# Kernel tuning notes

Measured on AMD Instinct MI355X. Metric: run time of the kernel, lower is better.

The kernel has to match this reference:

```python
import jax, jax.numpy as jnp
import numpy as np

B, T, D = 2, 2048, 512
H, W = 8, 32
d = D // H


def setup_inputs() -> dict:
    key = jax.random.key(0)
    ks = jax.random.split(key, 9)
    s = 1.0 / np.sqrt(D)
    return {
        "x": jax.random.normal(ks[0], (B, T, D), dtype=jnp.float32),
        "wq": jax.random.normal(ks[1], (D, D), dtype=jnp.float32) * s,
        "bq": jnp.zeros((D,), dtype=jnp.float32),
        "wk": jax.random.normal(ks[2], (D, D), dtype=jnp.float32) * s,
        "bk": jnp.zeros((D,), dtype=jnp.float32),
        "wv": jax.random.normal(ks[3], (D, D), dtype=jnp.float32) * s,
        "bv": jnp.zeros((D,), dtype=jnp.float32),
        "wo": jax.random.normal(ks[4], (D, D), dtype=jnp.float32) * s,
        "bo": jnp.zeros((D,), dtype=jnp.float32),
    }


def _local_attn(x, wq, bq, wk, bk, wv, bv, wo, bo):
    Bx, Tx, Dx = x.shape
    # projections (weights stored as [D_in, D_out])
    Q = (x @ wq + bq).reshape(Bx, Tx, H, d).transpose(0, 2, 1, 3)  # [B,H,T,d]
    K = (x @ wk + bk).reshape(Bx, Tx, H, d).transpose(0, 2, 1, 3)
    V = (x @ wv + bv).reshape(Bx, Tx, H, d).transpose(0, 2, 1, 3)
    # zero-pad time axis by W on both sides (matches F.pad value=0; NO masking,
    # padded zero keys get score 0 and participate in softmax like the original)
    Kp = jnp.pad(K, ((0, 0), (0, 0), (W, W), (0, 0)))  # [B,H,T+2W,d]
    Vp = jnp.pad(V, ((0, 0), (0, 0), (W, W), (0, 0)))
    idx = jnp.arange(Tx)[:, None] + jnp.arange(2 * W + 1)[None, :]  # [T, 2W+1]
    K_loc = Kp[:, :, idx, :]  # [B,H,T,2W+1,d]
    V_loc = Vp[:, :, idx, :]
    scores = jnp.einsum("bhtd,bhtwd->bhtw", Q, K_loc) / jnp.sqrt(jnp.asarray(d, x.dtype))
    attn = jax.nn.softmax(scores, axis=-1)
    out = jnp.einsum("bhtw,bhtwd->bhtd", attn, V_loc)  # [B,H,T,d]
    out = out.transpose(0, 2, 1, 3).reshape(Bx, Tx, Dx)
    return out @ wo + bo


def reference(x, wq, bq, wk, bk, wv, bv, wo, bo):
    return _local_attn(x, wq, bq, wk, bk, wv, bv, wo, bo)
```

## Files before the change

kernel.cpp:

```cpp
#include <hip/hip_runtime.h>

using f16x8 = __attribute__((ext_vector_type(8))) _Float16;
using f16x4 = __attribute__((ext_vector_type(4))) _Float16;
using f32x4 = __attribute__((ext_vector_type(4))) float;

#define T_SEQ 2048
#define D_MODEL 512
#define NH 8
#define HD 64
#define NB 2
#define M_ROWS (NB * T_SEQ)

#define GLOAD_LDS16(g, l)                                              \
  __builtin_amdgcn_global_load_lds(                                    \
      (const __attribute__((address_space(1))) void*)(g),              \
      (__attribute__((address_space(3))) void*)(l), 16, 0, 0)

__global__ __launch_bounds__(256) void cvt_w(
    const float* __restrict__ wq, const float* __restrict__ wk,
    const float* __restrict__ wv, const float* __restrict__ wo,
    const float* __restrict__ bq, const float* __restrict__ bk,
    const float* __restrict__ bv, _Float16* __restrict__ wT,
    float* __restrict__ bias3) {
  const int z = blockIdx.z;
  const float* w = z == 0 ? wq : z == 1 ? wk : z == 2 ? wv : wo;
  __shared__ float t[32][33];
  int r0 = blockIdx.y * 32, c0 = blockIdx.x * 32;
  int i = threadIdx.x;
#pragma unroll
  for (int p = 0; p < 4; ++p) {
    int e = p * 256 + i;
    int row = e >> 5, col = e & 31;
    t[row][col] = w[(size_t)(r0 + row) * D_MODEL + c0 + col];
  }
  __syncthreads();
  _Float16* o = wT + (size_t)z * D_MODEL * D_MODEL;
#pragma unroll
  for (int p = 0; p < 4; ++p) {
    int e = p * 256 + i;
    int orow = e >> 5, ocol = e & 31;
    o[(size_t)(c0 + orow) * D_MODEL + r0 + ocol] = (_Float16)t[ocol][orow];
  }
  if (blockIdx.x == 0 && blockIdx.y == 0 && z < 3) {
    const float* bb = z == 0 ? bq : z == 1 ? bk : bv;
#pragma unroll
    for (int p = 0; p < 2; ++p)
      bias3[z * D_MODEL + p * 256 + i] = bb[p * 256 + i];
  }
}

template <int OUT_F32, int BM, int AF32>
__global__ __launch_bounds__(256) void gemm_bt(
    const void* __restrict__ Abase, const _Float16* __restrict__ BtBase,
    const float* __restrict__ biasBase, void* outBase) {
  constexpr int BN = 128;
  constexpr int WROWS = (BM >= 128) ? 2 : 1;
  constexpr int WCOLS = 4 / WROWS;
  constexpr int MF = BM / WROWS / 16;
  constexpr int NF = BN / WCOLS / 16;
  constexpr int NT = D_MODEL / 32;
  const int z = blockIdx.z;
  const _Float16* Bt = BtBase + (size_t)z * D_MODEL * D_MODEL;
  const float* bias = biasBase + z * D_MODEL;
  const int m0 = blockIdx.y * BM;
  const int n0 = blockIdx.x * BN;
  __shared__ _Float16 At[2][BM * 32];
  __shared__ _Float16 Bts[2][BN * 32];
  const int tid = threadIdx.x;
  const int l = tid & 63;
  const int wv = tid >> 6;
  const int wm = wv / WCOLS, wn = wv % WCOLS;
  const int r16 = l & 15, g4 = l >> 4;
  f32x4 acc[MF][NF] = {};
  const float* Af = (const float*)Abase;
  const _Float16* Ah = (const _Float16*)Abase;

  float4 ar[2][2];

  auto loadA = [&](int k0) {
#pragma unroll
    for (int cc = 0; cc < BM / 64; ++cc) {
      int c = tid + cc * 256;
      int row = c >> 2, part = c & 3;
      const float* src = &Af[(size_t)(m0 + row) * D_MODEL + k0 + part * 8];
      ar[cc][0] = *(const float4*)src;
      ar[cc][1] = *(const float4*)(src + 4);
    }
  };
  auto writeA = [&](int bb) {
#pragma unroll
    for (int cc = 0; cc < BM / 64; ++cc) {
      int c = tid + cc * 256;
      f16x8 h;
#pragma unroll
      for (int j = 0; j < 4; ++j) {
        h[j] = (_Float16)ar[cc][0][j];
        h[4 + j] = (_Float16)ar[cc][1][j];
      }
      *(f16x8*)&At[bb][c * 8] = h;
    }
  };
  auto stageA16 = [&](int bb, int k0) {
#pragma unroll
    for (int cc = 0; cc < BM / 64; ++cc) {
      int c = tid + cc * 256;
      int row = c >> 2, part = c & 3;
      GLOAD_LDS16(&Ah[(size_t)(m0 + row) * D_MODEL + k0 + part * 8],
                  &At[bb][(c - l) * 8]);
    }
  };
  auto stageB = [&](int bb, int k0) {
#pragma unroll
    for (int cc = 0; cc < BN / 64; ++cc) {
      int c = tid + cc * 256;
      int row = c >> 2, part = c & 3;
      GLOAD_LDS16(&Bt[(size_t)(n0 + row) * D_MODEL + k0 + part * 8],
                  &Bts[bb][(c - l) * 8]);
    }
  };
  auto compute = [&](int bb) {
    f16x8 a[MF], b[NF];
#pragma unroll
    for (int mf = 0; mf < MF; ++mf)
      a[mf] = *(const f16x8*)&At[bb][(wm * (BM / WROWS) + mf * 16 + r16) * 32 +
                                     g4 * 8];
#pragma unroll
    for (int nf = 0; nf < NF; ++nf)
      b[nf] = *(const f16x8*)&Bts[bb][(wn * (BN / WCOLS) + nf * 16 + r16) * 32 +
                                      g4 * 8];
#pragma unroll
    for (int mf = 0; mf < MF; ++mf)
#pragma unroll
      for (int nf = 0; nf < NF; ++nf)
        acc[mf][nf] = __builtin_amdgcn_mfma_f32_16x16x32_f16(
            a[mf], b[nf], acc[mf][nf], 0, 0, 0);
  };

  if constexpr (AF32) {
    loadA(0);
    stageB(0, 0);
    writeA(0);
  } else {
    stageA16(0, 0);
    stageB(0, 0);
  }
  __syncthreads();
#pragma unroll
  for (int t = 0; t < NT; ++t) {
    if constexpr (AF32) {
      if (t + 1 < NT) {
        loadA((t + 1) * 32);
        stageB((t + 1) & 1, (t + 1) * 32);
      }
      compute(t & 1);
      if (t + 1 < NT) writeA((t + 1) & 1);
    } else {
      if (t + 1 < NT) {
        stageA16((t + 1) & 1, (t + 1) * 32);
        stageB((t + 1) & 1, (t + 1) * 32);
      }
      compute(t & 1);
    }
    __syncthreads();
  }

#pragma unroll
  for (int mf = 0; mf < MF; ++mf) {
#pragma unroll
    for (int nf = 0; nf < NF; ++nf) {
      int col = n0 + wn * (BN / WCOLS) + nf * 16 + r16;
      float bs = bias[col];
#pragma unroll
      for (int r = 0; r < 4; ++r) {
        int rowi = m0 + wm * (BM / WROWS) + mf * 16 + g4 * 4 + r;
        float v = acc[mf][nf][r] + bs;
        if (OUT_F32)
          ((float*)outBase)[(size_t)rowi * D_MODEL + col] = v;
        else
          ((_Float16*)outBase)[(size_t)z * M_ROWS * D_MODEL +
                               (size_t)rowi * D_MODEL + col] = (_Float16)v;
      }
    }
  }
}

__global__ __launch_bounds__(256) void local_attn(
    const _Float16* __restrict__ Q, const _Float16* __restrict__ K,
    const _Float16* __restrict__ V, _Float16* __restrict__ att) {
  const int t0 = blockIdx.x * 64;
  const int h = blockIdx.y;
  const int b = blockIdx.z;
  const int k0 = t0 - 32;
  __shared__ _Float16 Ks[128 * 64];
  __shared__ _Float16 Vt[64 * 136];
  __shared__ _Float16 Ps[64 * 136];
  const int tid = threadIdx.x;
  const int l = tid & 63;
  const int wv = tid >> 6;
  const int r16 = l & 15, g4 = l >> 4;
  const size_t colbase = (size_t)h * HD;
  f16x8 qf[2];
#pragma unroll
  for (int kk = 0; kk < 2; ++kk)
    qf[kk] = *(const f16x8*)&Q[(size_t)(b * T_SEQ + t0 + wv * 16 + r16) *
                                   D_MODEL + colbase + kk * 32 + g4 * 8];
  const bool interior = (k0 >= 0) && (k0 + 128 <= T_SEQ);
  if (interior) {
#pragma unroll
    for (int cc = 0; cc < 4; ++cc) {
      int c = tid + cc * 256;
      int row = c >> 3, part = c & 7;
      int sp = part ^ (row & 7);
      GLOAD_LDS16(
          &K[(size_t)(b * T_SEQ + k0 + row) * D_MODEL + colbase + sp * 8],
          &Ks[(c - l) * 8]);
    }
  } else {
#pragma unroll
    for (int cc = 0; cc < 4; ++cc) {
      int c = tid + cc * 256;
      int row = c >> 3, part = c & 7;
      int t = k0 + row;
      f16x8 v = {};
      if (t >= 0 && t < T_SEQ)
        v = *(const f16x8*)&K[(size_t)(b * T_SEQ + t) * D_MODEL + colbase +
                              part * 8];
      *(f16x8*)&Ks[row * 64 + (part ^ (row & 7)) * 8] = v;
    }
  }
#pragma unroll
  for (int cc = 0; cc < 4; ++cc) {
    int c = tid + cc * 256;
    int row = c >> 3, part = c & 7;
    int t = k0 + row;
    f16x8 v = {};
    if (t >= 0 && t < T_SEQ)
      v = *(const f16x8*)&V[(size_t)(b * T_SEQ + t) * D_MODEL + colbase +
                            part * 8];
#pragma unroll
    for (int j = 0; j < 8; ++j) Vt[(part * 8 + j) * 136 + row] = v[j];
  }
  __syncthreads();
  f32x4 s[8] = {};
#pragma unroll
  for (int kk = 0; kk < 2; ++kk) {
    int p = kk * 4 + g4;
#pragma unroll
    for (int nf = 0; nf < 8; ++nf) {
      f16x8 bb =
          *(const f16x8*)&Ks[(nf * 16 + r16) * 64 + (p ^ (r16 & 7)) * 8];
      s[nf] = __builtin_amdgcn_mfma_f32_16x16x32_f16(qf[kk], bb, s[nf], 0, 0, 0);
    }
  }
#pragma unroll
  for (int r = 0; r < 4; ++r) {
    int ql = wv * 16 + g4 * 4 + r;
    float vals[8];
    float m = -1e30f;
#pragma unroll
    for (int nf = 0; nf < 8; ++nf) {
      int j = nf * 16 + r16;
      bool in = (j >= ql) && (j <= ql + 64);
      float sv = in ? s[nf][r] * 0.125f : -1e30f;
      vals[nf] = sv;
      m = fmaxf(m, sv);
    }
#pragma unroll
    for (int off = 1; off < 16; off <<= 1) m = fmaxf(m, __shfl_xor(m, off, 64));
    float e[8];
    float sum = 0.f;
#pragma unroll
    for (int nf = 0; nf < 8; ++nf) {
      float ev = (vals[nf] > -1e29f) ? __expf(vals[nf] - m) : 0.f;
      e[nf] = ev;
      sum += ev;
    }
#pragma unroll
    for (int off = 1; off < 16; off <<= 1) sum += __shfl_xor(sum, off, 64);
    float inv = 1.f / sum;
#pragma unroll
    for (int nf = 0; nf < 8; ++nf)
      Ps[ql * 136 + nf * 16 + r16] = (_Float16)(e[nf] * inv);
  }
  __syncthreads();
  f32x4 o[4] = {};
#pragma unroll
  for (int kk = 0; kk < 4; ++kk) {
    f16x8 a = *(const f16x8*)&Ps[(wv * 16 + r16) * 136 + kk * 32 + g4 * 8];
#pragma unroll
    for (int nf = 0; nf < 4; ++nf) {
      f16x8 bb = *(const f16x8*)&Vt[(nf * 16 + r16) * 136 + kk * 32 + g4 * 8];
      o[nf] = __builtin_amdgcn_mfma_f32_16x16x32_f16(a, bb, o[nf], 0, 0, 0);
    }
  }
#pragma unroll
  for (int nf = 0; nf < 4; ++nf)
#pragma unroll
    for (int r = 0; r < 4; ++r) {
      int row = t0 + wv * 16 + g4 * 4 + r;
      int col = nf * 16 + r16;
      att[(size_t)(b * T_SEQ + row) * D_MODEL + colbase + col] =
          (_Float16)o[nf][r];
    }
}

extern "C" void kernel_launch(void* const* d_in, const int* in_sizes, int n_in,
                              void* d_out, int out_size, void* d_ws,
                              size_t ws_size, hipStream_t stream) {
  const float* x = (const float*)d_in[0];
  const float* wq = (const float*)d_in[1];
  const float* bq = (const float*)d_in[2];
  const float* wk = (const float*)d_in[3];
  const float* bk = (const float*)d_in[4];
  const float* wv = (const float*)d_in[5];
  const float* bv = (const float*)d_in[6];
  const float* wo = (const float*)d_in[7];
  const float* bo = (const float*)d_in[8];

  char* ws = (char*)d_ws;
  _Float16* wT = (_Float16*)(ws);
  float* bias3 = (float*)(ws + (2 << 20));
  _Float16* QKV = (_Float16*)(ws + (4 << 20));
  _Float16* att = (_Float16*)(ws + (16 << 20));

  cvt_w<<<dim3(16, 16, 4), 256, 0, stream>>>(wq, wk, wv, wo, bq, bk, bv, wT,
                                             bias3);
  gemm_bt<0, 128, 1><<<dim3(4, 32, 3), 256, 0, stream>>>(x, wT, bias3, QKV);
  const _Float16* Qm = QKV;
  const _Float16* Km = QKV + (size_t)M_ROWS * D_MODEL;
  const _Float16* Vm = Km + (size_t)M_ROWS * D_MODEL;
  local_attn<<<dim3(32, 8, 2), 256, 0, stream>>>(Qm, Km, Vm, att);
  gemm_bt<1, 64, 0><<<dim3(4, 64, 1), 256, 0, stream>>>(
      att, wT + (size_t)3 * D_MODEL * D_MODEL, bo, d_out);
}
```

Measured before the change: 48.71 us.

## Fuse weight conversion into QKV GEMM with flag sync and triple-buffered pipelines

Removes the separate weight-conversion kernel. In the QKV GEMM kernel, the blocks in row ny==0 transpose their slice of wq/wk/wv to fp16 and publish a per-slice flag; every block spin-waits on that flag before its GEMM. The wo transpose moves into the first 256 blocks of the attention kernel. Both GEMMs now use triple-buffered LDS with explicit vmcnt waits and XOR-swizzled LDS layouts to cut bank conflicts and launch overhead. The cross-block spin-wait could deadlock if waiting blocks fill the device before the producer blocks run, and the flags add a memset per call.

Measured after the change: 127.0 us. +160.8%, slower.

```diff
diff --git a/kernel.cpp b/kernel.cpp
--- a/kernel.cpp
+++ b/kernel.cpp
@@ -16,185 +16,189 @@
       (const __attribute__((address_space(1))) void*)(g),              \
       (__attribute__((address_space(3))) void*)(l), 16, 0, 0)
 
-__global__ __launch_bounds__(256) void cvt_w(
-    const float* __restrict__ wq, const float* __restrict__ wk,
-    const float* __restrict__ wv, const float* __restrict__ wo,
+__global__ __launch_bounds__(256) void k_qkvw(
+    const float* __restrict__ x, const float* __restrict__ wq,
+    const float* __restrict__ wk, const float* __restrict__ wv,
     const float* __restrict__ bq, const float* __restrict__ bk,
     const float* __restrict__ bv, _Float16* __restrict__ wT,
-    float* __restrict__ bias3) {
-  const int z = blockIdx.z;
-  const float* w = z == 0 ? wq : z == 1 ? wk : z == 2 ? wv : wo;
-  __shared__ float t[32][33];
-  int r0 = blockIdx.y * 32, c0 = blockIdx.x * 32;
-  int i = threadIdx.x;
-#pragma unroll
-  for (int p = 0; p < 4; ++p) {
-    int e = p * 256 + i;
-    int row = e >> 5, col = e & 31;
-    t[row][col] = w[(size_t)(r0 + row) * D_MODEL + c0 + col];
+    _Float16* __restrict__ QKV, int* __restrict__ flags) {
+  __shared__ __align__(16) char smraw[49152];
+  const int nx = blockIdx.x, ny = blockIdx.y, z = blockIdx.z;
+  const float* w = z == 0 ? wq : z == 1 ? wk : wv;
+  const float* bias = z == 0 ? bq : z == 1 ? bk : bv;
+  _Float16* wTz = wT + (size_t)z * D_MODEL * D_MODEL;
+  const int p = z * 4 + nx;
+  const int n0 = nx * 128, m0 = ny * 128;
+  const int tid = threadIdx.x;
+
+  if (ny == 0) {
+    float* Lf = (float*)smraw;
+    for (int k0 = 0; k0 < D_MODEL; k0 += 64) {
+      __syncthreads();
+#pragma unroll
+      for (int u = 0; u < 8; ++u) {
+        int c = tid + u * 256;
+        int row = c >> 5, ncl = (c & 31) * 4;
+        *(float4*)&Lf[row * 136 + ncl] =
+            *(const float4*)&w[(size_t)(k0 + row) * D_MODEL + n0 + ncl];
+      }
+      __syncthreads();
+#pragma unroll
+      for (int u = 0; u < 4; ++u) {
+        int F = tid + u * 256;
+        int n = F >> 3, kq = F & 7;
+        f16x8 h;
+#pragma unroll
+        for (int j = 0; j < 8; ++j)
+          h[j] = (_Float16)Lf[(kq * 8 + j) * 136 + n];
+        *(f16x8*)&wTz[(size_t)(n0 + n) * D_MODEL + k0 + kq * 8] = h;
+      }
+    }
+    __threadfence();
+    __syncthreads();
+    if (tid == 0)
+      __hip_atomic_store(&flags[p], 1, __ATOMIC_RELEASE,
+                         __HIP_MEMORY_SCOPE_AGENT);
+  }
+  if (tid == 0) {
+    while (!__hip_atomic_load(&flags[p], __ATOMIC_ACQUIRE,
+                              __HIP_MEMORY_SCOPE_AGENT))
+      __builtin_amdgcn_s_sleep(16);
   }
   __syncthreads();
-  _Float16* o = wT + (size_t)z * D_MODEL * D_MODEL;
-#pragma unroll
-  for (int p = 0; p < 4; ++p) {
-    int e = p * 256 + i;
-    int orow = e >> 5, ocol = e & 31;
-    o[(size_t)(c0 + orow) * D_MODEL + r0 + ocol] = (_Float16)t[ocol][orow];
-  }
-  if (blockIdx.x == 0 && blockIdx.y == 0 && z < 3) {
-    const float* bb = z == 0 ? bq : z == 1 ? bk : bv;
-#pragma unroll
-    for (int p = 0; p < 2; ++p)
-      bias3[z * D_MODEL + p * 256 + i] = bb[p * 256 + i];
-  }
-}
-
-template <int OUT_F32, int BM, int AF32>
-__global__ __launch_bounds__(256) void gemm_bt(
-    const void* __restrict__ Abase, const _Float16* __restrict__ BtBase,
-    const float* __restrict__ biasBase, void* outBase) {
-  constexpr int BN = 128;
-  constexpr int WROWS = (BM >= 128) ? 2 : 1;
-  constexpr int WCOLS = 4 / WROWS;
-  constexpr int MF = BM / WROWS / 16;
-  constexpr int NF = BN / WCOLS / 16;
+
   constexpr int NT = D_MODEL / 32;
-  const int z = blockIdx.z;
-  const _Float16* Bt = BtBase + (size_t)z * D_MODEL * D_MODEL;
-  const float* bias = biasBase + z * D_MODEL;
-  const int m0 = blockIdx.y * BM;
-  const int n0 = blockIdx.x * BN;
-  __shared__ _Float16 At[2][BM * 32];
-  __shared__ _Float16 Bts[2][BN * 32];
-  const int tid = threadIdx.x;
+  _Float16* At = (_Float16*)smraw;
+  _Float16* Bts = (_Float16*)(smraw + 24576);
   const int l = tid & 63;
-  const int wv = tid >> 6;
-  const int wm = wv / WCOLS, wn = wv % WCOLS;
+  const int wvv = tid >> 6;
+  const int wm = wvv >> 1, wn = wvv & 1;
   const int r16 = l & 15, g4 = l >> 4;
-  f32x4 acc[MF][NF] = {};
-  const float* Af = (const float*)Abase;
-  const _Float16* Ah = (const _Float16*)Abase;
-
+  f32x4 acc[4][4] = {};
   float4 ar[2][2];
 
   auto loadA = [&](int k0) {
 #pragma unroll
-    for (int cc = 0; cc < BM / 64; ++cc) {
+    for (int cc = 0; cc < 2; ++cc) {
       int c = tid + cc * 256;
       int row = c >> 2, part = c & 3;
-      const float* src = &Af[(size_t)(m0 + row) * D_MODEL + k0 + part * 8];
+      const float* src = &x[(size_t)(m0 + row) * D_MODEL + k0 + part * 8];
       ar[cc][0] = *(const float4*)src;
       ar[cc][1] = *(const float4*)(src + 4);
     }
   };
   auto writeA = [&](int bb) {
 #pragma unroll
-    for (int cc = 0; cc < BM / 64; ++cc) {
-      int c = tid + cc * 256;
+    for (int cc = 0; cc < 2; ++cc) {
+      int c = tid + cc * 256;
+      int row = c >> 2, part = c & 3;
       f16x8 h;
 #pragma unroll
       for (int j = 0; j < 4; ++j) {
         h[j] = (_Float16)ar[cc][0][j];
         h[4 + j] = (_Float16)ar[cc][1][j];
       }
-      *(f16x8*)&At[bb][c * 8] = h;
-    }
-  };
-  auto stageA16 = [&](int bb, int k0) {
-#pragma unroll
-    for (int cc = 0; cc < BM / 64; ++cc) {
-      int c = tid + cc * 256;
-      int row = c >> 2, part = c & 3;
-      GLOAD_LDS16(&Ah[(size_t)(m0 + row) * D_MODEL + k0 + part * 8],
-                  &At[bb][(c - l) * 8]);
+      *(f16x8*)&At[bb * 4096 + row * 32 + ((part ^ (row & 3))) * 8] = h;
     }
   };
   auto stageB = [&](int bb, int k0) {
 #pragma unroll
-    for (int cc = 0; cc < BN / 64; ++cc) {
-      int c = tid + cc * 256;
-      int row = c >> 2, part = c & 3;
-      GLOAD_LDS16(&Bt[(size_t)(n0 + row) * D_MODEL + k0 + part * 8],
-                  &Bts[bb][(c - l) * 8]);
+    for (int cc = 0; cc < 2; ++cc) {
+      int c = tid + cc * 256;
+      int row = c >> 2, sp = (c & 3) ^ (row & 3);
+      GLOAD_LDS16(&wTz[(size_t)(n0 + row) * D_MODEL + k0 + sp * 8],
+                  &Bts[bb * 4096 + (c - l) * 8]);
     }
   };
   auto compute = [&](int bb) {
-    f16x8 a[MF], b[NF];
-#pragma unroll
-    for (int mf = 0; mf < MF; ++mf)
-      a[mf] = *(const f16x8*)&At[bb][(wm * (BM / WROWS) + mf * 16 + r16) * 32 +
-                                     g4 * 8];
-#pragma unroll
-    for (int nf = 0; nf < NF; ++nf)
-      b[nf] = *(const f16x8*)&Bts[bb][(wn * (BN / WCOLS) + nf * 16 + r16) * 32 +
-                                      g4 * 8];
-#pragma unroll
-    for (int mf = 0; mf < MF; ++mf)
-#pragma unroll
-      for (int nf = 0; nf < NF; ++nf)
+    f16x8 a[4], b[4];
+#pragma unroll
+    for (int mf = 0; mf < 4; ++mf) {
+      int row = wm * 64 + mf * 16 + r16;
+      a[mf] = *(const f16x8*)&At[bb * 4096 + row * 32 + (g4 ^ (row & 3)) * 8];
+    }
+#pragma unroll
+    for (int nf = 0; nf < 4; ++nf) {
+      int row = wn * 64 + nf * 16 + r16;
+      b[nf] = *(const f16x8*)&Bts[bb * 4096 + row * 32 + (g4 ^ (row & 3)) * 8];
+    }
+#pragma unroll
+    for (int mf = 0; mf < 4; ++mf)
+#pragma unroll
+      for (int nf = 0; nf < 4; ++nf)
         acc[mf][nf] = __builtin_amdgcn_mfma_f32_16x16x32_f16(
             a[mf], b[nf], acc[mf][nf], 0, 0, 0);
   };
 
-  if constexpr (AF32) {
-    loadA(0);
-    stageB(0, 0);
-    writeA(0);
-  } else {
-    stageA16(0, 0);
-    stageB(0, 0);
-  }
-  __syncthreads();
+  loadA(0);
+  stageB(0, 0);
+  asm volatile("s_waitcnt vmcnt(2)" ::: "memory");
+  writeA(0);
+  loadA(32);
+  stageB(1, 32);
 #pragma unroll
   for (int t = 0; t < NT; ++t) {
-    if constexpr (AF32) {
-      if (t + 1 < NT) {
-        loadA((t + 1) * 32);
-        stageB((t + 1) & 1, (t + 1) * 32);
+    if (t + 1 < NT)
+      asm volatile("s_waitcnt vmcnt(6)" ::: "memory");
+    else
+      asm volatile("s_waitcnt vmcnt(0)" ::: "memory");
+    asm volatile("s_waitcnt lgkmcnt(0)" ::: "memory");
+    __builtin_amdgcn_s_barrier();
+    if (t + 1 < NT) writeA((t + 1) % 3);
+    compute(t % 3);
+    if (t + 2 < NT) {
+      loadA((t + 2) * 32);
+      stageB((t + 2) % 3, (t + 2) * 32);
+    }
+  }
+
+#pragma unroll
+  for (int mf = 0; mf < 4; ++mf) {
+#pragma unroll
+    for (int nf = 0; nf < 4; ++nf) {
+      int col = n0 + wn * 64 + nf * 16 + r16;
+      float bs = bias[col];
+#pragma unroll
+      for (int r = 0; r < 4; ++r) {
+        int rowi = m0 + wm * 64 + mf * 16 + g4 * 4 + r;
+        QKV[(size_t)z * M_ROWS * D_MODEL + (size_t)rowi * D_MODEL + col] =
+            (_Float16)(acc[mf][nf][r] + bs);
       }
-      compute(t & 1);
-      if (t + 1 < NT) writeA((t + 1) & 1);
-    } else {
-      if (t + 1 < NT) {
-        stageA16((t + 1) & 1, (t + 1) * 32);
-        stageB((t + 1) & 1, (t + 1) * 32);
-      }
-      compute(t & 1);
-    }
-    __syncthreads();
-  }
-
-#pragma unroll
-  for (int mf = 0; mf < MF; ++mf) {
-#pragma unroll
-    for (int nf = 0; nf < NF; ++nf) {
-      int col = n0 + wn * (BN / WCOLS) + nf * 16 + r16;
-      float bs = bias[col];
-#pragma unroll
-      for (int r = 0; r < 4; ++r) {
-        int rowi = m0 + wm * (BM / WROWS) + mf * 16 + g4 * 4 + r;
-        float v = acc[mf][nf][r] + bs;
-        if (OUT_F32)
-          ((float*)outBase)[(size_t)rowi * D_MODEL + col] = v;
-        else
-          ((_Float16*)outBase)[(size_t)z * M_ROWS * D_MODEL +
-                               (size_t)rowi * D_MODEL + col] = (_Float16)v;
-      }
     }
   }
 }
 
-__global__ __launch_bounds__(256) void local_attn(
+__global__ __launch_bounds__(256) void k_attn(
     const _Float16* __restrict__ Q, const _Float16* __restrict__ K,
-    const _Float16* __restrict__ V, _Float16* __restrict__ att) {
+    const _Float16* __restrict__ V, const float* __restrict__ wo,
+    _Float16* __restrict__ woT, _Float16* __restrict__ att) {
+  __shared__ __align__(16) char smraw[51200];
   const int t0 = blockIdx.x * 64;
   const int h = blockIdx.y;
   const int b = blockIdx.z;
+  const int tid = threadIdx.x;
+  const int u = blockIdx.x + 32 * blockIdx.y + 256 * blockIdx.z;
+  if (u < 256) {
+    float(*t)[33] = (float(*)[33])smraw;
+    int r0 = (u >> 4) * 32, c0 = (u & 15) * 32;
+#pragma unroll
+    for (int pp = 0; pp < 4; ++pp) {
+      int e = pp * 256 + tid;
+      t[e >> 5][e & 31] = wo[(size_t)(r0 + (e >> 5)) * D_MODEL + c0 + (e & 31)];
+    }
+    __syncthreads();
+#pragma unroll
+    for (int pp = 0; pp < 4; ++pp) {
+      int e = pp * 256 + tid;
+      woT[(size_t)(c0 + (e >> 5)) * D_MODEL + r0 + (e & 31)] =
+          (_Float16)t[e & 31][e >> 5];
+    }
+    __syncthreads();
+  }
+  _Float16* Ks = (_Float16*)smraw;
+  _Float16* Vt = (_Float16*)(smraw + 16384);
+  _Float16* Ps = (_Float16*)(smraw + 16384 + 17408);
   const int k0 = t0 - 32;
-  __shared__ _Float16 Ks[128 * 64];
-  __shared__ _Float16 Vt[64 * 136];
-  __shared__ _Float16 Ps[64 * 136];
-  const int tid = threadIdx.x;
   const int l = tid & 63;
   const int wv = tid >> 6;
   const int r16 = l & 15, g4 = l >> 4;
@@ -244,12 +248,13 @@
   f32x4 s[8] = {};
 #pragma unroll
   for (int kk = 0; kk < 2; ++kk) {
-    int p = kk * 4 + g4;
+    int pp = kk * 4 + g4;
 #pragma unroll
     for (int nf = 0; nf < 8; ++nf) {
       f16x8 bb =
-          *(const f16x8*)&Ks[(nf * 16 + r16) * 64 + (p ^ (r16 & 7)) * 8];
-      s[nf] = __builtin_amdgcn_mfma_f32_16x16x32_f16(qf[kk], bb, s[nf], 0, 0, 0);
+          *(const f16x8*)&Ks[(nf * 16 + r16) * 64 + (pp ^ (r16 & 7)) * 8];
+      s[nf] =
+          __builtin_amdgcn_mfma_f32_16x16x32_f16(qf[kk], bb, s[nf], 0, 0, 0);
     }
   }
 #pragma unroll
@@ -302,6 +307,92 @@
       att[(size_t)(b * T_SEQ + row) * D_MODEL + colbase + col] =
           (_Float16)o[nf][r];
     }
+}
+
+__global__ __launch_bounds__(256) void k_out(
+    const _Float16* __restrict__ A, const _Float16* __restrict__ Bt,
+    const float* __restrict__ bias, float* __restrict__ out) {
+  constexpr int BM = 64, BN = 128;
+  constexpr int NT = D_MODEL / 32;
+  constexpr int LPS = BM / 64 + BN / 64;
+  __shared__ __align__(16) char smraw[36864];
+  _Float16* At = (_Float16*)smraw;
+  _Float16* Bts = (_Float16*)(smraw + 12288);
+  const int m0 = blockIdx.y * BM;
+  const int n0 = blockIdx.x * BN;
+  const int tid = threadIdx.x;
+  const int l = tid & 63;
+  const int wv = tid >> 6;
+  const int r16 = l & 15, g4 = l >> 4;
+  f32x4 acc[4][4] = {};
+
+  auto stage = [&](int bb, int k0) {
+    {
+      int c = tid;
+      int row = c >> 2, sp = (c & 3) ^ (row & 3);
+      GLOAD_LDS16(&A[(size_t)(m0 + row) * D_MODEL + k0 + sp * 8],
+                  &At[bb * BM * 32 + (c - l) * 8]);
+    }
+#pragma unroll
+    for (int cc = 0; cc < 2; ++cc) {
+      int c = tid + cc * 256;
+      int row = c >> 2, sp = (c & 3) ^ (row & 3);
+      GLOAD_LDS16(&Bt[(size_t)(n0 + row) * D_MODEL + k0 + sp * 8],
+                  &Bts[bb * BN * 32 + (c - l) * 8]);
+    }
+  };
+  auto compute = [&](int bb) {
+    f16x8 a[4], b[4];
+#pragma unroll
+    for (int mf = 0; mf < 4; ++mf) {
+      int row = mf * 16 + r16;
+      a[mf] = *(const f16x8*)&At[bb * 64 * 32 + row * 32 + (g4 ^ (row & 3)) * 8];
+    }
+#pragma unroll
+    for (int nf = 0; nf < 4; ++nf) {
+      int row = wv * 32 + (nf & 1) * 16 + r16 + (nf >> 1) * 0;
+      (void)row;
+    }
+#pragma unroll
+    for (int nf = 0; nf < 2; ++nf) {
+      int row = wv * 32 + nf * 16 + r16;
+      b[nf] = *(const f16x8*)&Bts[bb * 128 * 32 + row * 32 +
+                                  (g4 ^ (row & 3)) * 8];
+    }
+#pragma unroll
+    for (int mf = 0; mf < 4; ++mf)
+#pragma unroll
+      for (int nf = 0; nf < 2; ++nf)
+        acc[mf][nf] = __builtin_amdgcn_mfma_f32_16x16x32_f16(
+            a[mf], b[nf], acc[mf][nf], 0, 0, 0);
+  };
+
+  stage(0, 0);
+  stage(1, 32);
+#pragma unroll
+  for (int t = 0; t < NT; ++t) {
+    if (t + 1 < NT)
+      asm volatile("s_waitcnt vmcnt(%0)" ::"n"(LPS) : "memory");
+    else
+      asm volatile("s_waitcnt vmcnt(0)" ::: "memory");
+    __builtin_amdgcn_s_barrier();
+    compute(t % 3);
+    if (t + 2 < NT) stage((t + 2) % 3, (t + 2) * 32);
+  }
+
+#pragma unroll
+  for (int mf = 0; mf < 4; ++mf) {
+#pragma unroll
+    for (int nf = 0; nf < 2; ++nf) {
+      int col = n0 + wv * 32 + nf * 16 + r16;
+      float bs = bias[col];
+#pragma unroll
+      for (int r = 0; r < 4; ++r) {
+        int rowi = m0 + mf * 16 + g4 * 4 + r;
+        out[(size_t)rowi * D_MODEL + col] = acc[mf][nf][r] + bs;
+      }
+    }
+  }
 }
 
 extern "C" void kernel_launch(void* const* d_in, const int* in_sizes, int n_in,
@@ -316,20 +407,21 @@
   const float* bv = (const float*)d_in[6];
   const float* wo = (const float*)d_in[7];
   const float* bo = (const float*)d_in[8];
+  float* out = (float*)d_out;
 
   char* ws = (char*)d_ws;
   _Float16* wT = (_Float16*)(ws);
-  float* bias3 = (float*)(ws + (2 << 20));
+  _Float16* woT = (_Float16*)(ws + (2 << 20));
   _Float16* QKV = (_Float16*)(ws + (4 << 20));
   _Float16* att = (_Float16*)(ws + (16 << 20));
-
-  cvt_w<<<dim3(16, 16, 4), 256, 0, stream>>>(wq, wk, wv, wo, bq, bk, bv, wT,
-                                             bias3);
-  gemm_bt<0, 128, 1><<<dim3(4, 32, 3), 256, 0, stream>>>(x, wT, bias3, QKV);
+  int* flags = (int*)(ws + (20 << 20));
+
+  hipMemsetAsync(flags, 0, 64, stream);
+  k_qkvw<<<dim3(4, 32, 3), 256, 0, stream>>>(x, wq, wk, wv, bq, bk, bv, wT,
+                                             QKV, flags);
   const _Float16* Qm = QKV;
   const _Float16* Km = QKV + (size_t)M_ROWS * D_MODEL;
   const _Float16* Vm = Km + (size_t)M_ROWS * D_MODEL;
-  local_attn<<<dim3(32, 8, 2), 256, 0, stream>>>(Qm, Km, Vm, att);
-  gemm_bt<1, 64, 0><<<dim3(4, 64, 1), 256, 0, stream>>>(
-      att, wT + (size_t)3 * D_MODEL * D_MODEL, bo, d_out);
+  k_attn<<<dim3(32, 8, 2), 256, 0, stream>>>(Qm, Km, Vm, wo, woT, att);
+  k_out<<<dim3(4, 64), 256, 0, stream>>>(att, woT, bo, out);
 }
```
